# Performance work log

Hardware: AMD Instinct MI355X
Metric: run time of the kernel (lower is better)

Reference implementation:

```python
import jax, jax.numpy as jnp
import numpy as np

N_HEAD = 16

def setup_inputs() -> dict:
    key = jax.random.key(0)
    ks = jax.random.split(key, 5)
    B, T, D = 2, 2048, 1024
    BN = 1024  # bottleneck_dim
    s = 0.02
    return {
        "x": jax.random.normal(ks[0], (B, T, D), dtype=jnp.float32),
        "w_qkv": jax.random.normal(ks[1], (3 * BN, D), dtype=jnp.float32) * s,
        "b_qkv": jax.random.normal(ks[2], (3 * BN,), dtype=jnp.float32) * s,
        "w_proj": jax.random.normal(ks[3], (D, BN), dtype=jnp.float32) * s,
        "b_proj": jax.random.normal(ks[4], (D,), dtype=jnp.float32) * s,
        "top_k": 64,
    }

def reference(x, w_qkv, b_qkv, w_proj, b_proj, top_k):
    B, T, D = x.shape
    H = N_HEAD
    BN = w_qkv.shape[0] // 3
    Dh = BN // H
    # qkv projection; torch Linear: y = x @ W^T + b
    qkv = (x @ w_qkv.T + b_qkv).reshape(B, T, 3, H, Dh)
    q = jnp.moveaxis(qkv[:, :, 0], 1, 2)  # (B,H,T,Dh)
    k = jnp.moveaxis(qkv[:, :, 1], 1, 2)
    v = jnp.moveaxis(qkv[:, :, 2], 1, 2)
    att = jnp.einsum('bhqd,bhkd->bhqk', q, k) * (1.0 / np.sqrt(Dh).astype(np.float32))
    # SparseK mask: keep only top-k scores per query row, mask rest before softmax
    topv = jax.lax.top_k(att, top_k)[0]          # (B,H,T,top_k)
    thresh = topv[..., -1:]                      # kth largest per row
    att = jnp.where(att >= thresh, att, -jnp.inf)
    att = jax.nn.softmax(att, axis=-1)
    y = jnp.einsum('bhqk,bhkd->bhqd', att, v)    # (B,H,T,Dh)
    y = y.transpose(0, 2, 1, 3).reshape(B, T, BN)
    return y @ w_proj.T + b_proj
```

## Files before the change

kernel.cpp:

```cpp
#include <hip/hip_runtime.h>
#include <hip/hip_bf16.h>
#include <math.h>

#define Bz 2
#define Tz 2048
#define Dz 1024
#define Hz 16
#define DHz 64
#define BNz 1024
#define TOPKz 64
#define QBLK 16
#define CAND_MAX 176
#define BAND 8e-5f
#define SLO  -20.0f
#define SBINW 0.15625f
#define SBINR 6.4f
#define LDSB 40

typedef __attribute__((ext_vector_type(8))) short bf16x8;
typedef __attribute__((ext_vector_type(4))) short s16x4;
typedef __attribute__((ext_vector_type(4))) float f32x4;

__device__ __forceinline__ short f2bf(float f) {
  unsigned u = __float_as_uint(f);
  return (short)((u + 0x7FFFu + ((u >> 16) & 1u)) >> 16);
}
__device__ __forceinline__ float bf2f(short b) {
  return __uint_as_float(((unsigned)(unsigned short)b) << 16);
}
__device__ __forceinline__ unsigned f2s(float f) {
  unsigned u = __float_as_uint(f);
  return (u & 0x80000000u) ? ~u : (u | 0x80000000u);
}
__device__ __forceinline__ float s2f(unsigned u) {
  return __uint_as_float((u & 0x80000000u) ? (u & 0x7FFFFFFFu) : ~u);
}

__global__ __launch_bounds__(256) void qkv_gemm_split(
    const float* __restrict__ A, const float* __restrict__ W,
    const float* __restrict__ bias,
    float* __restrict__ q32, float* __restrict__ k32,
    short* __restrict__ kbf, float* __restrict__ v32)
{
  __shared__ __align__(16) short Ah[128][LDSB];
  __shared__ __align__(16) short Am[128][LDSB];
  __shared__ __align__(16) short Al[128][LDSB];
  __shared__ __align__(16) short Bh[64][LDSB];
  __shared__ __align__(16) short Bm[64][LDSB];
  __shared__ __align__(16) short Bl[64][LDSB];

  const int tid = threadIdx.x;
  const int lane = tid & 63, wid = tid >> 6;
  const int m0 = blockIdx.y * 128, n0 = blockIdx.x * 64;
  const int bcol = lane & 15, lgrp = lane >> 4;

  f32x4 acch[2][4], accl[2][4];
#pragma unroll
  for (int ms = 0; ms < 2; ++ms)
#pragma unroll
    for (int nt = 0; nt < 4; ++nt) {
      acch[ms][nt] = (f32x4){0.f, 0.f, 0.f, 0.f};
      accl[ms][nt] = (f32x4){0.f, 0.f, 0.f, 0.f};
    }

  const int arow = tid >> 1, ak = (tid & 1) * 16;
  const int brow = tid >> 2, bk = (tid & 3) * 8;
  const float* Ald = A + (size_t)(m0 + arow) * Dz + ak;
  const float* Wld = W + (size_t)(n0 + brow) * Dz + bk;

  for (int kt = 0; kt < Dz; kt += 32) {
    float4 a4[4], b4[2];
#pragma unroll
    for (int j = 0; j < 4; ++j) a4[j] = *(const float4*)(Ald + kt + 4*j);
#pragma unroll
    for (int j = 0; j < 2; ++j) b4[j] = *(const float4*)(Wld + kt + 4*j);
    __syncthreads();

#pragma unroll
    for (int j = 0; j < 4; ++j) {
      float vv[4] = {a4[j].x, a4[j].y, a4[j].z, a4[j].w};
      s16x4 h4, m4, l4;
#pragma unroll
      for (int e = 0; e < 4; ++e) {
        short hh = f2bf(vv[e]);
        float r1 = vv[e] - bf2f(hh);
        short mm = f2bf(r1);
        float r2 = r1 - bf2f(mm);
        h4[e] = hh; m4[e] = mm; l4[e] = f2bf(r2);
      }
      *(s16x4*)&Ah[arow][ak + 4*j] = h4;
      *(s16x4*)&Am[arow][ak + 4*j] = m4;
      *(s16x4*)&Al[arow][ak + 4*j] = l4;
    }
#pragma unroll
    for (int j = 0; j < 2; ++j) {
      float vv[4] = {b4[j].x, b4[j].y, b4[j].z, b4[j].w};
      s16x4 h4, m4, l4;
#pragma unroll
      for (int e = 0; e < 4; ++e) {
        short hh = f2bf(vv[e]);
        float r1 = vv[e] - bf2f(hh);
        short mm = f2bf(r1);
        float r2 = r1 - bf2f(mm);
        h4[e] = hh; m4[e] = mm; l4[e] = f2bf(r2);
      }
      *(s16x4*)&Bh[brow][bk + 4*j] = h4;
      *(s16x4*)&Bm[brow][bk + 4*j] = m4;
      *(s16x4*)&Bl[brow][bk + 4*j] = l4;
    }
    __syncthreads();

    bf16x8 ah[2], am[2], al[2];
#pragma unroll
    for (int ms = 0; ms < 2; ++ms) {
      int rr = wid*32 + ms*16 + bcol;
      ah[ms] = *(const bf16x8*)&Ah[rr][lgrp*8];
      am[ms] = *(const bf16x8*)&Am[rr][lgrp*8];
      al[ms] = *(const bf16x8*)&Al[rr][lgrp*8];
    }
#pragma unroll
    for (int nt = 0; nt < 4; ++nt) {
      int nr = nt*16 + bcol;
      bf16x8 bh = *(const bf16x8*)&Bh[nr][lgrp*8];
      bf16x8 bm = *(const bf16x8*)&Bm[nr][lgrp*8];
      bf16x8 bl = *(const bf16x8*)&Bl[nr][lgrp*8];
#pragma unroll
      for (int ms = 0; ms < 2; ++ms) {
        acch[ms][nt] = __builtin_amdgcn_mfma_f32_16x16x32_bf16(ah[ms], bh, acch[ms][nt], 0, 0, 0);
        accl[ms][nt] = __builtin_amdgcn_mfma_f32_16x16x32_bf16(ah[ms], bm, accl[ms][nt], 0, 0, 0);
        accl[ms][nt] = __builtin_amdgcn_mfma_f32_16x16x32_bf16(am[ms], bh, accl[ms][nt], 0, 0, 0);
        accl[ms][nt] = __builtin_amdgcn_mfma_f32_16x16x32_bf16(am[ms], bm, accl[ms][nt], 0, 0, 0);
        accl[ms][nt] = __builtin_amdgcn_mfma_f32_16x16x32_bf16(ah[ms], bl, accl[ms][nt], 0, 0, 0);
        accl[ms][nt] = __builtin_amdgcn_mfma_f32_16x16x32_bf16(al[ms], bh, accl[ms][nt], 0, 0, 0);
      }
    }
  }

#pragma unroll
  for (int ms = 0; ms < 2; ++ms)
#pragma unroll
    for (int nt = 0; nt < 4; ++nt)
#pragma unroll
      for (int rv = 0; rv < 4; ++rv) {
        int m = m0 + wid*32 + ms*16 + lgrp*4 + rv;
        int n = n0 + nt*16 + bcol;
        double val = (double)acch[ms][nt][rv] + (double)accl[ms][nt][rv] + (double)bias[n];
        int bb = m >> 11;
        int t = m & 2047;
        if (n < BNz) {
          int h = n >> 6, d = n & 63;
          q32[(((size_t)(bb*Hz + h))*Tz + t)*DHz + d] = (float)val;
        } else if (n < 2*BNz) {
          int h = (n - BNz) >> 6, d = n & 63;
          size_t bh = (size_t)(bb*Hz + h);
          float vf = (float)val;
          k32[(bh*Tz + t)*DHz + d] = vf;
          kbf[(bh*Tz + t)*DHz + d] = f2bf(vf);
        } else {
          int h = (n - 2*BNz) >> 6, d = n & 63;
          v32[(((size_t)(bb*Hz + h))*Tz + t)*DHz + d] = (float)val;
        }
      }
}

__global__ __launch_bounds__(256) void proj_gemm(
    const float* __restrict__ A, const float* __restrict__ W,
    const float* __restrict__ bias, float* __restrict__ out)
{
  __shared__ float As[16][68];
  __shared__ float Ws[16][68];
  const int tid = threadIdx.x;
  const int tx = tid & 15, ty = tid >> 4;
  const int m0 = blockIdx.y * 64, n0 = blockIdx.x * 64;
  const int lrow = tid >> 2, lkq = tid & 3;
  float acc[4][4] = {};
  const float* Aload = A + (size_t)(m0 + lrow) * Dz + lkq * 4;
  const float* Wload = W + (size_t)(n0 + lrow) * Dz + lkq * 4;
  for (int kt = 0; kt < Dz; kt += 16) {
    float4 a4 = *(const float4*)(Aload + kt);
    float4 w4 = *(const float4*)(Wload + kt);
    __syncthreads();
    As[lkq*4+0][lrow] = a4.x; As[lkq*4+1][lrow] = a4.y;
    As[lkq*4+2][lrow] = a4.z; As[lkq*4+3][lrow] = a4.w;
    Ws[lkq*4+0][lrow] = w4.x; Ws[lkq*4+1][lrow] = w4.y;
    Ws[lkq*4+2][lrow] = w4.z; Ws[lkq*4+3][lrow] = w4.w;
    __syncthreads();
#pragma unroll
    for (int k = 0; k < 16; ++k) {
      float4 av = *(const float4*)&As[k][ty*4];
      float4 wv = *(const float4*)&Ws[k][tx*4];
      float a_[4] = {av.x, av.y, av.z, av.w};
      float w_[4] = {wv.x, wv.y, wv.z, wv.w};
#pragma unroll
      for (int i = 0; i < 4; ++i)
#pragma unroll
        for (int j = 0; j < 4; ++j)
          acc[i][j] = fmaf(a_[i], w_[j], acc[i][j]);
    }
  }
#pragma unroll
  for (int i = 0; i < 4; ++i) {
    int m = m0 + ty*4 + i;
#pragma unroll
    for (int j = 0; j < 4; ++j) {
      int n = n0 + tx*4 + j;
      out[(size_t)m * Dz + n] = acc[i][j] + bias[n];
    }
  }
}

__global__ __launch_bounds__(256) void attn_topk(
    const float* __restrict__ q32g, const float* __restrict__ k32g,
    const short* __restrict__ kbfg, const float* __restrict__ v32,
    float* __restrict__ y)
{
  __shared__ float q_s[QBLK][DHz];
  __shared__ __align__(16) unsigned char ubuf[QBLK*CAND_MAX*6];
  __shared__ int bstar_s[QBLK];
  __shared__ int candcnt[QBLK];

  unsigned* hist = (unsigned*)ubuf;
  float* candv = (float*)ubuf;
  unsigned short* candidx = (unsigned short*)(ubuf + QBLK*CAND_MAX*4);

  const int tid = threadIdx.x;
  const int bid0 = blockIdx.x;
  const int bh_f = (bid0 & 7) + 8 * (bid0 >> 10);
  const int qbf = (bid0 >> 3) & 127;
  const int h = bh_f & 15;
  const int bb = bh_f >> 4;
  const size_t bh = (size_t)(bb * Hz + h);
  const float* qg = q32g + (bh * Tz + (size_t)qbf * QBLK) * DHz;
  const float* kg32 = k32g + bh * Tz * DHz;
  const short* kb = kbfg + bh * Tz * DHz;
  const float* vg = v32 + bh * Tz * DHz;

  if (tid < QBLK) candcnt[tid] = 0;
  for (int i = tid; i < QBLK*256; i += 256) hist[i] = 0u;
  {
    int r = tid >> 4, d4 = (tid & 15) * 4;
    *(float4*)&q_s[r][d4] = *(const float4*)&qg[r*DHz + d4];
  }
  __syncthreads();

  const int lane = tid & 63;
  const int wid = tid >> 6;
  const int bcol = lane & 15;
  const int lgrp = lane >> 4;
  bf16x8 aF0, aF1;
#pragma unroll
  for (int e = 0; e < 8; ++e) {
    aF0[e] = f2bf(q_s[bcol][lgrp*8 + e]);
    aF1[e] = f2bf(q_s[bcol][32 + lgrp*8 + e]);
  }
  const int t0base = wid * 512;

  unsigned binreg[32];
#pragma unroll 4
  for (int tt = 0; tt < 32; ++tt) {
    const short* kbp = kb + (size_t)(t0base + tt*16 + bcol) * DHz;
    bf16x8 b0 = *(const bf16x8*)(kbp + lgrp*8);
    bf16x8 b1 = *(const bf16x8*)(kbp + 32 + lgrp*8);
    f32x4 c = {0.f, 0.f, 0.f, 0.f};
    c = __builtin_amdgcn_mfma_f32_16x16x32_bf16(aF0, b0, c, 0, 0, 0);
    c = __builtin_amdgcn_mfma_f32_16x16x32_bf16(aF1, b1, c, 0, 0, 0);
    unsigned bw = 0u;
#pragma unroll
    for (int j = 0; j < 4; ++j) {
      int bin = (int)((c[j] - SLO) * SBINR);
      bin = bin < 0 ? 0 : (bin > 255 ? 255 : bin);
      atomicAdd(&hist[(lgrp*4 + j)*256 + bin], 1u);
      bw |= ((unsigned)bin) << (8*j);
    }
    binreg[tt] = bw;
  }
  __syncthreads();

  {
    int r = tid >> 4, i16 = tid & 15;
    int s = 0;
#pragma unroll
    for (int j = 0; j < 16; ++j) s += (int)hist[r*256 + i16*16 + j];
    int S = s;
#pragma unroll
    for (int off = 1; off < 16; off <<= 1) {
      int src = i16 + off;
      int v = __shfl(S, (lane & 48) | (src < 16 ? src : 15));
      S += (src < 16) ? v : 0;
    }
    unsigned long long blt = __ballot(S >= TOPKz);
    unsigned mask16 = (unsigned)((blt >> (lane & 48)) & 0xFFFFull);
    int istar = 31 - __builtin_clz(mask16);
    if (i16 == istar) {
      int cum = S - s;
      int b = istar * 16;
      for (int j = 15; j >= 0; --j) {
        cum += (int)hist[r*256 + istar*16 + j];
        if (cum >= TOPKz) { b = istar*16 + j; break; }
      }
      bstar_s[r] = b;
    }
  }
  __syncthreads();

  {
    int bc[4];
#pragma unroll
    for (int j = 0; j < 4; ++j) {
      int b = bstar_s[lgrp*4 + j] - 1;
      bc[j] = b < 0 ? 0 : b;
    }
#pragma unroll
    for (int tt = 0; tt < 32; ++tt) {
      unsigned bw = binreg[tt];
#pragma unroll
      for (int j = 0; j < 4; ++j) {
        int bin = (int)((bw >> (8*j)) & 255u);
        if (bin >= bc[j]) {
          int r = lgrp*4 + j;
          int p = atomicAdd(&candcnt[r], 1);
          if (p < CAND_MAX) candidx[r*CAND_MAX + p] = (unsigned short)(t0base + tt*16 + bcol);
        }
      }
    }
  }
  __syncthreads();

  {
    const int r = tid >> 4, i16 = tid & 15;
    int n = candcnt[r]; if (n > CAND_MAX) n = CAND_MAX;

    for (int i = i16; i < n; i += 16) {
      int col = (int)candidx[r*CAND_MAX + i];
      const float* kpd = kg32 + (size_t)col * DHz;
      double s = 0.0;
#pragma unroll
      for (int d = 0; d < DHz; d += 4) {
        float4 k4 = *(const float4*)(kpd + d);
        s = fma((double)q_s[r][d+0], (double)k4.x, s);
        s = fma((double)q_s[r][d+1], (double)k4.y, s);
        s = fma((double)q_s[r][d+2], (double)k4.z, s);
        s = fma((double)q_s[r][d+3], (double)k4.w, s);
      }
      candv[r*CAND_MAX + i] = (float)s;
    }

    float myv[11];
    float mx = -3.0e38f;
#pragma unroll
    for (int j = 0; j < 11; ++j) {
      int i = i16 + j*16;
      float x = (i < n) ? candv[r*CAND_MAX + i] : -3.0e38f;
      myv[j] = x;
      mx = fmaxf(mx, x);
    }
#pragma unroll
    for (int m = 1; m < 16; m <<= 1) mx = fmaxf(mx, __shfl_xor(mx, m));

    float mn = 3.0e38f;
#pragma unroll
    for (int j = 0; j < 11; ++j) {
      int i = i16 + j*16;
      if (i < n) mn = fminf(mn, myv[j]);
    }
#pragma unroll
    for (int m = 1; m < 16; m <<= 1) mn = fminf(mn, __shfl_xor(mn, m));
    unsigned lo_u = f2s(mn);
    unsigned hi_u = f2s(mx) + 1u;
    while (hi_u - lo_u > 1u) {
      unsigned mid = lo_u + ((hi_u - lo_u) >> 1);
      float tv = s2f(mid);
      int cnt = 0;
#pragma unroll
      for (int j = 0; j < 11; ++j) cnt += (myv[j] >= tv) ? 1 : 0;
#pragma unroll
      for (int m = 1; m < 16; m <<= 1) cnt += __shfl_xor(cnt, m);
      if (cnt >= TOPKz) lo_u = mid; else hi_u = mid;
    }
    const float T = s2f(lo_u);

    int na = 0, nb = 0;
#pragma unroll
    for (int j = 0; j < 11; ++j) {
      float s = myv[j];
      if (s > T + BAND) na++;
      else if (s >= T - BAND) nb++;
    }
#pragma unroll
    for (int m = 1; m < 16; m <<= 1) {
      na += __shfl_xor(na, m);
      nb += __shfl_xor(nb, m);
    }
    const float wb = (float)(TOPKz - na) / (float)(nb > 0 ? nb : 1);

    float lsum = 0.f;
#pragma unroll
    for (int j = 0; j < 11; ++j) {
      int i = i16 + j*16;
      if (i < n) {
        float s = myv[j];
        float w = (s > T + BAND) ? 1.f : ((s >= T - BAND) ? wb : 0.f);
        float p = (w > 0.f) ? w * expf((s - mx) * 0.125f) : 0.f;
        candv[r*CAND_MAX + i] = p;
        lsum += p;
      }
    }
#pragma unroll
    for (int m = 1; m < 16; m <<= 1) lsum += __shfl_xor(lsum, m);
    const float rd = 1.0f / lsum;

    const int dg = i16 * 4;
    float4 o = make_float4(0.f, 0.f, 0.f, 0.f);
    for (int i = 0; i < n; ++i) {
      float p = candv[r*CAND_MAX + i];
      if (p > 0.f) {
        int idx = (int)candidx[r*CAND_MAX + i];
        float4 vv = *(const float4*)&vg[(size_t)idx*DHz + dg];
        float pw = p * rd;
        o.x = fmaf(pw, vv.x, o.x);
        o.y = fmaf(pw, vv.y, o.y);
        o.z = fmaf(pw, vv.z, o.z);
        o.w = fmaf(pw, vv.w, o.w);
      }
    }
    float* yo = y + ((size_t)bb*Tz + (size_t)qbf*QBLK + r) * BNz + h*DHz + dg;
    *(float4*)yo = o;
  }
}

extern "C" void kernel_launch(void* const* d_in, const int* in_sizes, int n_in,
                              void* d_out, int out_size, void* d_ws, size_t ws_size,
                              hipStream_t stream)
{
  const float* x      = (const float*)d_in[0];
  const float* w_qkv  = (const float*)d_in[1];
  const float* b_qkv  = (const float*)d_in[2];
  const float* w_proj = (const float*)d_in[3];
  const float* b_proj = (const float*)d_in[4];
  float* out = (float*)d_out;

  const size_t E = (size_t)Bz * Hz * Tz * DHz;
  float* q32  = (float*)d_ws;
  float* k32  = q32 + E;
  short* kbf  = (short*)(k32 + E);
  float* v32  = (float*)(kbf + E);
  float* y    = v32 + E;

  qkv_gemm_split<<<dim3((3*BNz)/64, (Bz*Tz)/128), 256, 0, stream>>>(x, w_qkv, b_qkv, q32, k32, kbf, v32);
  attn_topk<<<Bz*Hz*(Tz/QBLK), 256, 0, stream>>>(q32, k32, kbf, v32, y);
  proj_gemm<<<dim3(Dz/64, (Bz*Tz)/64), 256, 0, stream>>>(y, w_proj, b_proj, out);
}
```

Before: 735.2 us.

## Use split-bf16 MFMA for output projection, pad histogram stride, drop branch

Replaces the scalar FP32 output-projection GEMM with an MFMA kernel that splits each FP32 operand into three bf16 parts (high, mid, low) and accumulates six cross products to approximate FP32 accuracy on matrix cores, using a 128x64 tile. It also pads the per-row LDS histogram stride from 256 to 257 to reduce bank conflicts on the atomics, and removes the p>0 branch in the P·V accumulation loop. The split-bf16 path adds conversion work and some precision risk, and the branchless loop now loads V rows even for zero-weight candidates.

```diff
diff --git a/kernel.cpp b/kernel.cpp
--- a/kernel.cpp
+++ b/kernel.cpp
@@ -16,6 +16,7 @@
 #define SBINW 0.15625f
 #define SBINR 6.4f
 #define LDSB 40
+#define HSTR 257
 
 typedef __attribute__((ext_vector_type(8))) short bf16x8;
 typedef __attribute__((ext_vector_type(4))) short s16x4;
@@ -163,50 +164,114 @@
       }
 }
 
-__global__ __launch_bounds__(256) void proj_gemm(
+__global__ __launch_bounds__(256) void proj_gemm_split(
     const float* __restrict__ A, const float* __restrict__ W,
     const float* __restrict__ bias, float* __restrict__ out)
 {
-  __shared__ float As[16][68];
-  __shared__ float Ws[16][68];
+  __shared__ __align__(16) short Ah[128][LDSB];
+  __shared__ __align__(16) short Am[128][LDSB];
+  __shared__ __align__(16) short Al[128][LDSB];
+  __shared__ __align__(16) short Bh[64][LDSB];
+  __shared__ __align__(16) short Bm[64][LDSB];
+  __shared__ __align__(16) short Bl[64][LDSB];
+
   const int tid = threadIdx.x;
-  const int tx = tid & 15, ty = tid >> 4;
-  const int m0 = blockIdx.y * 64, n0 = blockIdx.x * 64;
-  const int lrow = tid >> 2, lkq = tid & 3;
-  float acc[4][4] = {};
-  const float* Aload = A + (size_t)(m0 + lrow) * Dz + lkq * 4;
-  const float* Wload = W + (size_t)(n0 + lrow) * Dz + lkq * 4;
-  for (int kt = 0; kt < Dz; kt += 16) {
-    float4 a4 = *(const float4*)(Aload + kt);
-    float4 w4 = *(const float4*)(Wload + kt);
+  const int lane = tid & 63, wid = tid >> 6;
+  const int m0 = blockIdx.y * 128, n0 = blockIdx.x * 64;
+  const int bcol = lane & 15, lgrp = lane >> 4;
+
+  f32x4 acch[2][4], accl[2][4];
+#pragma unroll
+  for (int ms = 0; ms < 2; ++ms)
+#pragma unroll
+    for (int nt = 0; nt < 4; ++nt) {
+      acch[ms][nt] = (f32x4){0.f, 0.f, 0.f, 0.f};
+      accl[ms][nt] = (f32x4){0.f, 0.f, 0.f, 0.f};
+    }
+
+  const int arow = tid >> 1, ak = (tid & 1) * 16;
+  const int brow = tid >> 2, bk = (tid & 3) * 8;
+  const float* Ald = A + (size_t)(m0 + arow) * Dz + ak;
+  const float* Wld = W + (size_t)(n0 + brow) * Dz + bk;
+
+  for (int kt = 0; kt < Dz; kt += 32) {
+    float4 a4[4], b4[2];
+#pragma unroll
+    for (int j = 0; j < 4; ++j) a4[j] = *(const float4*)(Ald + kt + 4*j);
+#pragma unroll
+    for (int j = 0; j < 2; ++j) b4[j] = *(const float4*)(Wld + kt + 4*j);
     __syncthreads();
-    As[lkq*4+0][lrow] = a4.x; As[lkq*4+1][lrow] = a4.y;
-    As[lkq*4+2][lrow] = a4.z; As[lkq*4+3][lrow] = a4.w;
-    Ws[lkq*4+0][lrow] = w4.x; Ws[lkq*4+1][lrow] = w4.y;
-    Ws[lkq*4+2][lrow] = w4.z; Ws[lkq*4+3][lrow] = w4.w;
+
+#pragma unroll
+    for (int j = 0; j < 4; ++j) {
+      float vv[4] = {a4[j].x, a4[j].y, a4[j].z, a4[j].w};
+      s16x4 h4, m4, l4;
+#pragma unroll
+      for (int e = 0; e < 4; ++e) {
+        short hh = f2bf(vv[e]);
+        float r1 = vv[e] - bf2f(hh);
+        short mm = f2bf(r1);
+        float r2 = r1 - bf2f(mm);
+        h4[e] = hh; m4[e] = mm; l4[e] = f2bf(r2);
+      }
+      *(s16x4*)&Ah[arow][ak + 4*j] = h4;
+      *(s16x4*)&Am[arow][ak + 4*j] = m4;
+      *(s16x4*)&Al[arow][ak + 4*j] = l4;
+    }
+#pragma unroll
+    for (int j = 0; j < 2; ++j) {
+      float vv[4] = {b4[j].x, b4[j].y, b4[j].z, b4[j].w};
+      s16x4 h4, m4, l4;
+#pragma unroll
+      for (int e = 0; e < 4; ++e) {
+        short hh = f2bf(vv[e]);
+        float r1 = vv[e] - bf2f(hh);
+        short mm = f2bf(r1);
+        float r2 = r1 - bf2f(mm);
+        h4[e] = hh; m4[e] = mm; l4[e] = f2bf(r2);
+      }
+      *(s16x4*)&Bh[brow][bk + 4*j] = h4;
+      *(s16x4*)&Bm[brow][bk + 4*j] = m4;
+      *(s16x4*)&Bl[brow][bk + 4*j] = l4;
+    }
     __syncthreads();
-#pragma unroll
-    for (int k = 0; k < 16; ++k) {
-      float4 av = *(const float4*)&As[k][ty*4];
-      float4 wv = *(const float4*)&Ws[k][tx*4];
-      float a_[4] = {av.x, av.y, av.z, av.w};
-      float w_[4] = {wv.x, wv.y, wv.z, wv.w};
-#pragma unroll
-      for (int i = 0; i < 4; ++i)
-#pragma unroll
-        for (int j = 0; j < 4; ++j)
-          acc[i][j] = fmaf(a_[i], w_[j], acc[i][j]);
-    }
-  }
-#pragma unroll
-  for (int i = 0; i < 4; ++i) {
-    int m = m0 + ty*4 + i;
-#pragma unroll
-    for (int j = 0; j < 4; ++j) {
-      int n = n0 + tx*4 + j;
-      out[(size_t)m * Dz + n] = acc[i][j] + bias[n];
-    }
-  }
+
+    bf16x8 ah[2], am[2], al[2];
+#pragma unroll
+    for (int ms = 0; ms < 2; ++ms) {
+      int rr = wid*32 + ms*16 + bcol;
+      ah[ms] = *(const bf16x8*)&Ah[rr][lgrp*8];
+      am[ms] = *(const bf16x8*)&Am[rr][lgrp*8];
+      al[ms] = *(const bf16x8*)&Al[rr][lgrp*8];
+    }
+#pragma unroll
+    for (int nt = 0; nt < 4; ++nt) {
+      int nr = nt*16 + bcol;
+      bf16x8 bh = *(const bf16x8*)&Bh[nr][lgrp*8];
+      bf16x8 bm = *(const bf16x8*)&Bm[nr][lgrp*8];
+      bf16x8 bl = *(const bf16x8*)&Bl[nr][lgrp*8];
+#pragma unroll
+      for (int ms = 0; ms < 2; ++ms) {
+        acch[ms][nt] = __builtin_amdgcn_mfma_f32_16x16x32_bf16(ah[ms], bh, acch[ms][nt], 0, 0, 0);
+        accl[ms][nt] = __builtin_amdgcn_mfma_f32_16x16x32_bf16(ah[ms], bm, accl[ms][nt], 0, 0, 0);
+        accl[ms][nt] = __builtin_amdgcn_mfma_f32_16x16x32_bf16(am[ms], bh, accl[ms][nt], 0, 0, 0);
+        accl[ms][nt] = __builtin_amdgcn_mfma_f32_16x16x32_bf16(am[ms], bm, accl[ms][nt], 0, 0, 0);
+        accl[ms][nt] = __builtin_amdgcn_mfma_f32_16x16x32_bf16(ah[ms], bl, accl[ms][nt], 0, 0, 0);
+        accl[ms][nt] = __builtin_amdgcn_mfma_f32_16x16x32_bf16(al[ms], bh, accl[ms][nt], 0, 0, 0);
+      }
+    }
+  }
+
+#pragma unroll
+  for (int ms = 0; ms < 2; ++ms)
+#pragma unroll
+    for (int nt = 0; nt < 4; ++nt)
+#pragma unroll
+      for (int rv = 0; rv < 4; ++rv) {
+        int m = m0 + wid*32 + ms*16 + lgrp*4 + rv;
+        int n = n0 + nt*16 + bcol;
+        out[(size_t)m * Dz + n] = (acch[ms][nt][rv] + accl[ms][nt][rv]) + bias[n];
+      }
 }
 
 __global__ __launch_bounds__(256) void attn_topk(
@@ -236,7 +301,7 @@
   const float* vg = v32 + bh * Tz * DHz;
 
   if (tid < QBLK) candcnt[tid] = 0;
-  for (int i = tid; i < QBLK*256; i += 256) hist[i] = 0u;
+  for (int i = tid; i < QBLK*HSTR; i += 256) hist[i] = 0u;
   {
     int r = tid >> 4, d4 = (tid & 15) * 4;
     *(float4*)&q_s[r][d4] = *(const float4*)&qg[r*DHz + d4];
@@ -269,7 +334,7 @@
     for (int j = 0; j < 4; ++j) {
       int bin = (int)((c[j] - SLO) * SBINR);
       bin = bin < 0 ? 0 : (bin > 255 ? 255 : bin);
-      atomicAdd(&hist[(lgrp*4 + j)*256 + bin], 1u);
+      atomicAdd(&hist[(lgrp*4 + j)*HSTR + bin], 1u);
       bw |= ((unsigned)bin) << (8*j);
     }
     binreg[tt] = bw;
@@ -280,7 +345,7 @@
     int r = tid >> 4, i16 = tid & 15;
     int s = 0;
 #pragma unroll
-    for (int j = 0; j < 16; ++j) s += (int)hist[r*256 + i16*16 + j];
+    for (int j = 0; j < 16; ++j) s += (int)hist[r*HSTR + i16*16 + j];
     int S = s;
 #pragma unroll
     for (int off = 1; off < 16; off <<= 1) {
@@ -295,7 +360,7 @@
       int cum = S - s;
       int b = istar * 16;
       for (int j = 15; j >= 0; --j) {
-        cum += (int)hist[r*256 + istar*16 + j];
+        cum += (int)hist[r*HSTR + istar*16 + j];
         if (cum >= TOPKz) { b = istar*16 + j; break; }
       }
       bstar_s[r] = b;
@@ -413,15 +478,13 @@
     float4 o = make_float4(0.f, 0.f, 0.f, 0.f);
     for (int i = 0; i < n; ++i) {
       float p = candv[r*CAND_MAX + i];
-      if (p > 0.f) {
-        int idx = (int)candidx[r*CAND_MAX + i];
-        float4 vv = *(const float4*)&vg[(size_t)idx*DHz + dg];
-        float pw = p * rd;
-        o.x = fmaf(pw, vv.x, o.x);
-        o.y = fmaf(pw, vv.y, o.y);
-        o.z = fmaf(pw, vv.z, o.z);
-        o.w = fmaf(pw, vv.w, o.w);
-      }
+      int idx = (int)candidx[r*CAND_MAX + i];
+      float4 vv = *(const float4*)&vg[(size_t)idx*DHz + dg];
+      float pw = p * rd;
+      o.x = fmaf(pw, vv.x, o.x);
+      o.y = fmaf(pw, vv.y, o.y);
+      o.z = fmaf(pw, vv.z, o.z);
+      o.w = fmaf(pw, vv.w, o.w);
     }
     float* yo = y + ((size_t)bb*Tz + (size_t)qbf*QBLK + r) * BNz + h*DHz + dg;
     *(float4*)yo = o;
@@ -448,5 +511,5 @@
 
   qkv_gemm_split<<<dim3((3*BNz)/64, (Bz*Tz)/128), 256, 0, stream>>>(x, w_qkv, b_qkv, q32, k32, kbf, v32);
   attn_topk<<<Bz*Hz*(Tz/QBLK), 256, 0, stream>>>(q32, k32, kbf, v32, y);
-  proj_gemm<<<dim3(Dz/64, (Bz*Tz)/64), 256, 0, stream>>>(y, w_proj, b_proj, out);
-}
+  proj_gemm_split<<<dim3(Dz/64, (Bz*Tz)/128), 256, 0, stream>>>(y, w_proj, b_proj, out);
+}
```

After: 633.3 us. 1.16x faster.
